# Optimization experiments

Hardware: AMD Instinct MI355X
Metric: run time of the kernel (lower is better)

Reference implementation:

```python
import jax, jax.numpy as jnp
import numpy as np

NUM_HEADS = 12
THETA = 10000.0

def apply_rope(x, pos, theta):
    # x: [B, H, S, d_k]; pos: [S]
    d_k = x.shape[-1]
    inv_freq = theta ** (-jnp.arange(0, d_k, 2, dtype=jnp.float32) / d_k)  # [d_k/2]
    ang = pos[:, None].astype(jnp.float32) * inv_freq[None, :]             # [S, d_k/2]
    cos, sin = jnp.cos(ang), jnp.sin(ang)
    x1, x2 = x[..., ::2], x[..., 1::2]
    out_even = x1 * cos - x2 * sin
    out_odd = x1 * sin + x2 * cos
    # interleave back to [..., d_k]
    return jnp.stack([out_even, out_odd], axis=-1).reshape(x.shape)

def setup_inputs() -> dict:
    key = jax.random.key(0)
    ks = jax.random.split(key, 5)
    B, S, D = 1, 4096, 768
    x = jax.random.normal(ks[0], (B, S, D), dtype=jnp.float32)
    scale = 0.02
    Wq = jax.random.normal(ks[1], (D, D), dtype=jnp.float32) * scale
    Wk = jax.random.normal(ks[2], (D, D), dtype=jnp.float32) * scale
    Wv = jax.random.normal(ks[3], (D, D), dtype=jnp.float32) * scale
    Wo = jax.random.normal(ks[4], (D, D), dtype=jnp.float32) * scale
    return {"x": x, "Wq": Wq, "Wk": Wk, "Wv": Wv, "Wo": Wo}

def reference(x, Wq, Wk, Wv, Wo):
    B, S, D = x.shape
    H = NUM_HEADS
    d_k = D // H
    # projections (torch Linear: y = x @ W.T, no bias)
    Q = x @ Wq.T
    K = x @ Wk.T
    V = x @ Wv.T
    # [B, S, H*d_k] -> [B, H, S, d_k]
    def split_heads(t):
        return t.reshape(B, S, H, d_k).transpose(0, 2, 1, 3)
    Q, K, V = split_heads(Q), split_heads(K), split_heads(V)
    pos = jnp.arange(S)
    Q = apply_rope(Q, pos, THETA)
    K = apply_rope(K, pos, THETA)
    scores = jnp.einsum('bhnd,bhmd->bhnm', Q, K) * (d_k ** -0.5)  # [B,H,S,S]
    causal = jnp.tril(jnp.ones((S, S), dtype=bool))
    scores = jnp.where(causal, scores, -jnp.inf)
    attn = jax.nn.softmax(scores, axis=-1)
    out = jnp.einsum('bhnm,bhmd->bhnd', attn, V)  # [B,H,S,d_k]
    out = out.transpose(0, 2, 1, 3).reshape(B, S, D)
    return out @ Wo.T
```

## Files before the change

kernel.cpp:

```cpp
#include <hip/hip_runtime.h>
#include <hip/hip_bf16.h>
#include <cstdint>

typedef __bf16 bf16x8 __attribute__((ext_vector_type(8)));
typedef float f32x4 __attribute__((ext_vector_type(4)));
typedef float f32x16 __attribute__((ext_vector_type(16)));

static constexpr int S = 4096;
static constexpr int D = 768;
static constexpr int DK = 64;

__device__ __forceinline__ unsigned short f2bf(float f) {
  unsigned u = __float_as_uint(f);
  u = (u + 0x7fffu + ((u >> 16) & 1u)) >> 16;
  return (unsigned short)u;
}

__global__ __launch_bounds__(256) void cvt5_kernel(
    const float* __restrict__ x, const float* __restrict__ wq,
    const float* __restrict__ wk, const float* __restrict__ wv,
    const float* __restrict__ wo,
    unsigned short* __restrict__ xb, unsigned short* __restrict__ wqb,
    unsigned short* __restrict__ wkb, unsigned short* __restrict__ wvb,
    unsigned short* __restrict__ wob, float2* __restrict__ tab) {
  int i = blockIdx.x * blockDim.x + threadIdx.x;
  constexpr int NX4 = (S * D) / 4;
  constexpr int NW4 = (D * D) / 4;
  constexpr int NC = NX4 + 4 * NW4;
  if (i < NC) {
    const float* src;
    unsigned short* dst;
    int off;
    if (i < NX4)               { src = x;  dst = xb;  off = i; }
    else if (i < NX4 + NW4)    { src = wq; dst = wqb; off = i - NX4; }
    else if (i < NX4 + 2*NW4)  { src = wk; dst = wkb; off = i - NX4 - NW4; }
    else if (i < NX4 + 3*NW4)  { src = wv; dst = wvb; off = i - NX4 - 2*NW4; }
    else                       { src = wo; dst = wob; off = i - NX4 - 3*NW4; }
    float4 v = reinterpret_cast<const float4*>(src)[off];
    ushort4 o;
    o.x = f2bf(v.x); o.y = f2bf(v.y); o.z = f2bf(v.z); o.w = f2bf(v.w);
    reinterpret_cast<ushort4*>(dst)[off] = o;
  } else {
    int idx = i - NC;
    if (idx < S * 32) {
      int s = idx >> 5, ii = idx & 31;
      float freq = expf(-(float)(2 * ii) * (9.210340371976184f / 64.0f));
      float si, c;
      sincosf((float)s * freq, &si, &c);
      tab[idx] = make_float2(c, si);
    }
  }
}

__global__ __launch_bounds__(512) void qkv_gemm_kernel(
    const unsigned short* __restrict__ xb,
    const unsigned short* __restrict__ Wall,
    const float2* __restrict__ tab,
    unsigned short* __restrict__ Qh,
    unsigned short* __restrict__ Kf,
    unsigned short* __restrict__ Vf) {
  __shared__ alignas(16) unsigned short At[2][128 * 64];
  __shared__ alignas(16) unsigned short Bt[2][128 * 64];

  const int t = threadIdx.x;
  const int lane = t & 63;
  const int lr = lane & 15;
  const int hi = lane >> 4;
  const int wave = t >> 6;
  const int wr = wave >> 1, wc = wave & 1;
  const int row0 = blockIdx.x * 128;
  const int n0 = blockIdx.y * 128;
  const int sx = lr & 7;

  f32x4 acc[2][4] = {};

  auto stage = [&](int buf, int k0) {
#pragma unroll
    for (int j = 0; j < 2; ++j) {
      const int ci = wave * 128 + j * 64 + lane;
      const int row = ci >> 3;
      const int c16 = ci & 7;
      const int csrc = (c16 ^ (row & 7)) * 8;
      __builtin_amdgcn_global_load_lds(
          (const __attribute__((address_space(1))) void*)(
              xb + (size_t)(row0 + row) * 768 + k0 + csrc),
          (__attribute__((address_space(3))) void*)(&At[buf][row * 64 + c16 * 8]),
          16, 0, 0);
      __builtin_amdgcn_global_load_lds(
          (const __attribute__((address_space(1))) void*)(
              Wall + (size_t)(n0 + row) * 768 + k0 + csrc),
          (__attribute__((address_space(3))) void*)(&Bt[buf][row * 64 + c16 * 8]),
          16, 0, 0);
    }
  };

  stage(0, 0);
  __syncthreads();

#pragma unroll
  for (int ts = 0; ts < 12; ++ts) {
    const int cur = ts & 1;
    if (ts + 1 < 12) stage(cur ^ 1, (ts + 1) * 64);
#pragma unroll
    for (int kk = 0; kk < 2; ++kk) {
      const int csw = ((kk * 4 + hi) ^ sx) * 8;
      bf16x8 a[2], b[4];
#pragma unroll
      for (int rf = 0; rf < 2; ++rf)
        a[rf] = *reinterpret_cast<const bf16x8*>(
            &At[cur][(wr * 32 + rf * 16 + lr) * 64 + csw]);
#pragma unroll
      for (int nf = 0; nf < 4; ++nf)
        b[nf] = *reinterpret_cast<const bf16x8*>(
            &Bt[cur][(wc * 64 + nf * 16 + lr) * 64 + csw]);
#pragma unroll
      for (int rf = 0; rf < 2; ++rf)
#pragma unroll
        for (int nf = 0; nf < 4; ++nf)
          acc[rf][nf] = __builtin_amdgcn_mfma_f32_16x16x32_bf16(a[rf], b[nf], acc[rf][nf], 0, 0, 0);
    }
    __syncthreads();
  }

  const int z = n0 / 768;

  if (z < 2) {
#pragma unroll
    for (int nf = 0; nf < 4; ++nf) {
      const int c = n0 - z * 768 + wc * 64 + nf * 16 + lr;
      const int hh = c >> 6;
      const int dk = c & 63;
      const int ii = dk >> 1;
#pragma unroll
      for (int rf = 0; rf < 2; ++rf) {
        const int jrow = row0 + wr * 32 + rf * 16 + hi * 4;
#pragma unroll
        for (int j = 0; j < 4; ++j) {
          float v = acc[rf][nf][j];
          const int s = jrow + j;
          float pv = __shfl_xor(v, 1);
          float2 cs = tab[(size_t)s * 32 + ii];
          v = (dk & 1) ? (pv * cs.y + v * cs.x) : (v * cs.x - pv * cs.y);
          if (z == 0) {
            Qh[((size_t)hh * S + s) * DK + dk] = f2bf(v * 0.18033688f);
          } else {
            const size_t koff = ((size_t)hh * 128 + (s >> 5)) * 2048 +
                                (size_t)(dk >> 4) * 512 + ((dk >> 3) & 1) * 256 +
                                (s & 31) * 8 + (dk & 7);
            Kf[koff] = f2bf(v);
          }
        }
      }
    }
  } else {
#pragma unroll
    for (int nf = 0; nf < 4; ++nf) {
      const int c = n0 - 1536 + wc * 64 + nf * 16 + lr;
      const int hh = c >> 6;
      const int dv = c & 63;
#pragma unroll
      for (int rf = 0; rf < 2; ++rf) {
        const int jrow = row0 + wr * 32 + rf * 16 + hi * 4;
#pragma unroll
        for (int j = 0; j < 4; ++j) {
          const int s = jrow + j;
          const size_t voff = ((size_t)hh * 256 + (s >> 4)) * 1024 +
                              (size_t)(dv >> 5) * 512 + (dv & 31) * 16 +
                              ((s >> 3) & 1) * 8 + (s & 7);
          Vf[voff] = f2bf(acc[rf][nf][j]);
        }
      }
    }
  }
}

__global__ __launch_bounds__(256) void attn_kernel(
    const unsigned short* __restrict__ Qh,
    const unsigned short* __restrict__ Kf,
    const unsigned short* __restrict__ Vf,
    unsigned short* __restrict__ AO) {
  const int c = blockIdx.x;
  const int sslot = blockIdx.y;
  const int m3 = 3 * (c >> 1);
  const int g = sslot / 3, r = sslot - 3 * g;
  int h, qt;
  if ((c & 1) == 0) {
    if (r == 0)      { h = m3;     qt = 127 - 2 * g; }
    else if (r == 1) { h = m3 + 1; qt = 127 - 2 * g; }
    else             { h = m3;     qt = 126 - 2 * g; }
  } else {
    if (r == 0)      { h = m3 + 2; qt = 127 - 2 * g; }
    else if (r == 1) { h = m3 + 2; qt = 126 - 2 * g; }
    else             { h = m3 + 1; qt = 126 - 2 * g; }
  }

  const int wave = threadIdx.x >> 6;
  const int lane = threadIdx.x & 63;
  const int lq = lane & 31;
  const int hi2 = lane >> 5;
  const int q0w = qt * 32;
  const int qg = q0w + lq;

  const unsigned short* Qp = Qh + ((size_t)h * S + qg) * DK + hi2 * 8;
  const unsigned short* Kfp = Kf + (size_t)h * (S * DK) + hi2 * 256 + lq * 8;
  const unsigned short* Vfp = Vf + (size_t)h * (S * DK) + lq * 16 + hi2 * 8;

  bf16x8 qf[4];
#pragma unroll
  for (int ks = 0; ks < 4; ++ks)
    qf[ks] = *reinterpret_cast<const bf16x8*>(Qp + ks * 16);

  f32x16 acc0 = {}, acc1 = {};
  float lsum[16];
#pragma unroll
  for (int r2 = 0; r2 < 16; ++r2) lsum[r2] = 0.f;

  const int kvmax = ((q0w + 31) >> 6) << 6;
  const int kvfirst = 64 * wave;

  bf16x8 ka[2][4];
  if (kvfirst <= kvmax) {
    const unsigned short* K0 = Kfp + ((size_t)(kvfirst >> 5)) * 2048;
#pragma unroll
    for (int tt = 0; tt < 2; ++tt)
#pragma unroll
      for (int ks = 0; ks < 4; ++ks)
        ka[tt][ks] = *reinterpret_cast<const bf16x8*>(K0 + (size_t)tt * 2048 + ks * 512);
  }

  for (int kv0 = kvfirst; kv0 <= kvmax; kv0 += 256) {
    bf16x8 vb[2][4];
#pragma unroll
    for (int dvh = 0; dvh < 2; ++dvh)
#pragma unroll
      for (int ks = 0; ks < 4; ++ks)
        vb[dvh][ks] = *reinterpret_cast<const bf16x8*>(
            Vfp + ((size_t)(kv0 >> 4) + ks) * 1024 + dvh * 512);

    f32x16 s0 = {}, s1 = {};
#pragma unroll
    for (int ks = 0; ks < 4; ++ks) {
      s0 = __builtin_amdgcn_mfma_f32_32x32x16_bf16(ka[0][ks], qf[ks], s0, 0, 0, 0);
      s1 = __builtin_amdgcn_mfma_f32_32x32x16_bf16(ka[1][ks], qf[ks], s1, 0, 0, 0);
    }

    if ((kv0 + 256) <= kvmax) {
      const unsigned short* Kn = Kfp + ((size_t)((kv0 + 256) >> 5)) * 2048;
#pragma unroll
      for (int tt = 0; tt < 2; ++tt)
#pragma unroll
        for (int ks = 0; ks < 4; ++ks)
          ka[tt][ks] = *reinterpret_cast<const bf16x8*>(Kn + (size_t)tt * 2048 + ks * 512);
    }

    if ((kv0 + 63) > q0w) {
#pragma unroll
      for (int rr = 0; rr < 16; ++rr) {
        const int kvr = kv0 + (rr & 3) + 8 * (rr >> 2) + 4 * hi2;
        if (kvr > qg) s0[rr] = -1e30f;
        if (kvr + 32 > qg) s1[rr] = -1e30f;
      }
    }

#pragma unroll
    for (int rr = 0; rr < 16; ++rr) {
      float e0, e1;
      asm("v_exp_f32 %0, %1" : "=v"(e0) : "v"(s0[rr]));
      asm("v_exp_f32 %0, %1" : "=v"(e1) : "v"(s1[rr]));
      s0[rr] = e0;
      s1[rr] = e1;
      lsum[rr] += e0 + e1;
    }

    bf16x8 pa[4];
#pragma unroll
    for (int ks = 0; ks < 4; ++ks) {
      const int a4 = 8 * (ks & 1);
      unsigned X01, X23, Y01, Y23;
      if (ks < 2) {
        asm("v_cvt_pk_bf16_f32 %0, %1, %2" : "=v"(X01) : "v"(s0[a4 + 0]), "v"(s0[a4 + 1]));
        asm("v_cvt_pk_bf16_f32 %0, %1, %2" : "=v"(X23) : "v"(s0[a4 + 2]), "v"(s0[a4 + 3]));
        asm("v_cvt_pk_bf16_f32 %0, %1, %2" : "=v"(Y01) : "v"(s0[a4 + 4]), "v"(s0[a4 + 5]));
        asm("v_cvt_pk_bf16_f32 %0, %1, %2" : "=v"(Y23) : "v"(s0[a4 + 6]), "v"(s0[a4 + 7]));
      } else {
        asm("v_cvt_pk_bf16_f32 %0, %1, %2" : "=v"(X01) : "v"(s1[a4 + 0]), "v"(s1[a4 + 1]));
        asm("v_cvt_pk_bf16_f32 %0, %1, %2" : "=v"(X23) : "v"(s1[a4 + 2]), "v"(s1[a4 + 3]));
        asm("v_cvt_pk_bf16_f32 %0, %1, %2" : "=v"(Y01) : "v"(s1[a4 + 4]), "v"(s1[a4 + 5]));
        asm("v_cvt_pk_bf16_f32 %0, %1, %2" : "=v"(Y23) : "v"(s1[a4 + 6]), "v"(s1[a4 + 7]));
      }
      asm volatile("v_permlane32_swap_b32 %0, %1" : "+v"(X01), "+v"(Y01));
      asm volatile("v_permlane32_swap_b32 %0, %1" : "+v"(X23), "+v"(Y23));
      union { unsigned u[4]; bf16x8 v; } P;
      P.u[0] = X01; P.u[1] = X23; P.u[2] = Y01; P.u[3] = Y23;
      pa[ks] = P.v;
    }

#pragma unroll
    for (int ks = 0; ks < 4; ++ks) {
      acc0 = __builtin_amdgcn_mfma_f32_32x32x16_bf16(pa[ks], vb[0][ks], acc0, 0, 0, 0);
      acc1 = __builtin_amdgcn_mfma_f32_32x32x16_bf16(pa[ks], vb[1][ks], acc1, 0, 0, 0);
    }
  }

#pragma unroll
  for (int off = 8; off > 0; off >>= 1)
#pragma unroll
    for (int rr = 0; rr < 8; ++rr)
      if (rr < off) lsum[rr] += lsum[rr + off];
  const float l_ = lsum[0] + __shfl_xor(lsum[0], 32);

  __shared__ float llds[4][32];
  __shared__ float obuf[4][64][17];

  if (hi2 == 0) llds[wave][lq] = l_;

#pragma unroll
  for (int rr = 0; rr < 16; ++rr) obuf[wave][lane][rr] = acc0[rr];
  __syncthreads();

  const float Ltot = llds[0][lq] + llds[1][lq] + llds[2][lq] + llds[3][lq];
  const float linv = 1.0f / Ltot;

  float v0[4];
#pragma unroll
  for (int rr = 0; rr < 4; ++rr) {
    const int rq = wave * 4 + rr;
    v0[rr] = obuf[0][lane][rq] + obuf[1][lane][rq] + obuf[2][lane][rq] + obuf[3][lane][rq];
  }
  __syncthreads();

#pragma unroll
  for (int rr = 0; rr < 16; ++rr) obuf[wave][lane][rr] = acc1[rr];
  __syncthreads();

#pragma unroll
  for (int rr = 0; rr < 4; ++rr) {
    const int rq = wave * 4 + rr;
    const float v1 = obuf[0][lane][rq] + obuf[1][lane][rq] + obuf[2][lane][rq] + obuf[3][lane][rq];
    const int row = (rq & 3) + 8 * (rq >> 2) + 4 * hi2;
    const float li = __shfl(linv, row);
    const size_t s = q0w + row;
    AO[s * D + h * DK + lq]      = f2bf(v0[rr] * li);
    AO[s * D + h * DK + 32 + lq] = f2bf(v1 * li);
  }
}

__global__ __launch_bounds__(256) void oproj_kernel(
    const unsigned short* __restrict__ AO,
    const unsigned short* __restrict__ Wob,
    float* __restrict__ out) {
  __shared__ alignas(16) unsigned short At[2][64 * 64];
  __shared__ alignas(16) unsigned short Bt[2][128 * 64];

  const int t = threadIdx.x;
  const int lane = t & 63;
  const int lr = lane & 15;
  const int hi = lane >> 4;
  const int wave = t >> 6;
  const int wr = wave >> 1, wc = wave & 1;
  const int row0 = blockIdx.x * 64;
  const int n0 = blockIdx.y * 128;
  const int sx = lr & 7;

  f32x4 acc[2][4] = {};

  auto stage = [&](int buf, int k0) {
#pragma unroll
    for (int p = 0; p < 2; ++p) {
      const int ci = p * 256 + t;
      const int row = ci >> 3;
      const int c16 = ci & 7;
      const int csrc = (c16 ^ (row & 7)) * 8;
      __builtin_amdgcn_global_load_lds(
          (const __attribute__((address_space(1))) void*)(
              AO + (size_t)(row0 + row) * 768 + k0 + csrc),
          (__attribute__((address_space(3))) void*)(&At[buf][row * 64 + c16 * 8]),
          16, 0, 0);
    }
#pragma unroll
    for (int p = 0; p < 4; ++p) {
      const int ci = p * 256 + t;
      const int row = ci >> 3;
      const int c16 = ci & 7;
      const int csrc = (c16 ^ (row & 7)) * 8;
      __builtin_amdgcn_global_load_lds(
          (const __attribute__((address_space(1))) void*)(
              Wob + (size_t)(n0 + row) * 768 + k0 + csrc),
          (__attribute__((address_space(3))) void*)(&Bt[buf][row * 64 + c16 * 8]),
          16, 0, 0);
    }
  };

  stage(0, 0);
  __syncthreads();

#pragma unroll
  for (int ts = 0; ts < 12; ++ts) {
    const int cur = ts & 1;
    if (ts + 1 < 12) stage(cur ^ 1, (ts + 1) * 64);
#pragma unroll
    for (int kk = 0; kk < 2; ++kk) {
      const int csw = ((kk * 4 + hi) ^ sx) * 8;
      bf16x8 a[2], b[4];
#pragma unroll
      for (int rf = 0; rf < 2; ++rf)
        a[rf] = *reinterpret_cast<const bf16x8*>(
            &At[cur][(wr * 32 + rf * 16 + lr) * 64 + csw]);
#pragma unroll
      for (int nf = 0; nf < 4; ++nf)
        b[nf] = *reinterpret_cast<const bf16x8*>(
            &Bt[cur][(wc * 64 + nf * 16 + lr) * 64 + csw]);
#pragma unroll
      for (int rf = 0; rf < 2; ++rf)
#pragma unroll
        for (int nf = 0; nf < 4; ++nf)
          acc[rf][nf] = __builtin_amdgcn_mfma_f32_16x16x32_bf16(a[rf], b[nf], acc[rf][nf], 0, 0, 0);
    }
    __syncthreads();
  }

#pragma unroll
  for (int rf = 0; rf < 2; ++rf) {
    const int jrow = row0 + wr * 32 + rf * 16 + hi * 4;
#pragma unroll
    for (int nf = 0; nf < 4; ++nf) {
      const int cn = n0 + wc * 64 + nf * 16 + lr;
#pragma unroll
      for (int j = 0; j < 4; ++j)
        out[(size_t)(jrow + j) * D + cn] = acc[rf][nf][j];
    }
  }
}

extern "C" void kernel_launch(void* const* d_in, const int* in_sizes, int n_in,
                              void* d_out, int out_size, void* d_ws, size_t ws_size,
                              hipStream_t stream) {
  const float* x  = (const float*)d_in[0];
  const float* Wq = (const float*)d_in[1];
  const float* Wk = (const float*)d_in[2];
  const float* Wv = (const float*)d_in[3];
  const float* Wo = (const float*)d_in[4];
  float* out = (float*)d_out;

  char* ws = (char*)d_ws;
  unsigned short* xb  = (unsigned short*)(ws + 0);
  unsigned short* Wqb = (unsigned short*)(ws + 6291456);
  unsigned short* Wkb = (unsigned short*)(ws + 7471104);
  unsigned short* Wvb = (unsigned short*)(ws + 8650752);
  unsigned short* Wob = (unsigned short*)(ws + 9830400);
  unsigned short* Qh  = (unsigned short*)(ws + 11010048);
  unsigned short* Kf  = (unsigned short*)(ws + 17301504);
  unsigned short* Vf  = (unsigned short*)(ws + 23592960);
  unsigned short* AO  = (unsigned short*)(ws + 29884416);
  float2* tab = (float2*)(ws + 29884416);

  cvt5_kernel<<<5888, 256, 0, stream>>>(x, Wq, Wk, Wv, Wo, xb, Wqb, Wkb, Wvb, Wob, tab);
  qkv_gemm_kernel<<<dim3(32, 18), 512, 0, stream>>>(xb, Wqb, tab, Qh, Kf, Vf);
  attn_kernel<<<dim3(8, 192), 256, 0, stream>>>(Qh, Kf, Vf, AO);
  oproj_kernel<<<dim3(64, 6), 256, 0, stream>>>(AO, Wob, out);
}
```

Before: 98.43 us.

## Share K/V tiles across waves via LDS double buffering in attention

Each attention block now covers 128 query rows, one 32-row strip per wave, instead of splitting one 32-row strip's KV range across four waves. K and V tiles are staged into LDS with global_load_lds in a double buffer, so all four waves reuse each loaded tile. This removes the cross-wave reduction of partial outputs and row sums through shared memory at the end. In exchange the grid shrinks fourfold to 384 blocks and a block barrier is added per KV tile. Causal imbalance also grows, since waves in the same block stop at different KV tiles but still wait at every barrier.

```diff
diff --git a/kernel.cpp b/kernel.cpp
--- a/kernel.cpp
+++ b/kernel.cpp
@@ -183,27 +183,30 @@
   const int sslot = blockIdx.y;
   const int m3 = 3 * (c >> 1);
   const int g = sslot / 3, r = sslot - 3 * g;
-  int h, qt;
+  int h, qb;
   if ((c & 1) == 0) {
-    if (r == 0)      { h = m3;     qt = 127 - 2 * g; }
-    else if (r == 1) { h = m3 + 1; qt = 127 - 2 * g; }
-    else             { h = m3;     qt = 126 - 2 * g; }
+    if (r == 0)      { h = m3;     qb = 31 - 2 * g; }
+    else if (r == 1) { h = m3 + 1; qb = 31 - 2 * g; }
+    else             { h = m3;     qb = 30 - 2 * g; }
   } else {
-    if (r == 0)      { h = m3 + 2; qt = 127 - 2 * g; }
-    else if (r == 1) { h = m3 + 2; qt = 126 - 2 * g; }
-    else             { h = m3 + 1; qt = 126 - 2 * g; }
+    if (r == 0)      { h = m3 + 2; qb = 31 - 2 * g; }
+    else if (r == 1) { h = m3 + 2; qb = 30 - 2 * g; }
+    else             { h = m3 + 1; qb = 30 - 2 * g; }
   }
 
   const int wave = threadIdx.x >> 6;
   const int lane = threadIdx.x & 63;
   const int lq = lane & 31;
   const int hi2 = lane >> 5;
-  const int q0w = qt * 32;
+  const int q0w = qb * 128 + wave * 32;
   const int qg = q0w + lq;
 
   const unsigned short* Qp = Qh + ((size_t)h * S + qg) * DK + hi2 * 8;
-  const unsigned short* Kfp = Kf + (size_t)h * (S * DK) + hi2 * 256 + lq * 8;
-  const unsigned short* Vfp = Vf + (size_t)h * (S * DK) + lq * 16 + hi2 * 8;
+  const unsigned short* Kfp = Kf + (size_t)h * (S * DK);
+  const unsigned short* Vfp = Vf + (size_t)h * (S * DK);
+
+  __shared__ alignas(16) unsigned short Kt[2][4096];
+  __shared__ alignas(16) unsigned short Vt[2][4096];
 
   bf16x8 qf[4];
 #pragma unroll
@@ -215,91 +218,102 @@
 #pragma unroll
   for (int r2 = 0; r2 < 16; ++r2) lsum[r2] = 0.f;
 
-  const int kvmax = ((q0w + 31) >> 6) << 6;
-  const int kvfirst = 64 * wave;
-
-  bf16x8 ka[2][4];
-  if (kvfirst <= kvmax) {
-    const unsigned short* K0 = Kfp + ((size_t)(kvfirst >> 5)) * 2048;
-#pragma unroll
-    for (int tt = 0; tt < 2; ++tt)
-#pragma unroll
-      for (int ks = 0; ks < 4; ++ks)
-        ka[tt][ks] = *reinterpret_cast<const bf16x8*>(K0 + (size_t)tt * 2048 + ks * 512);
-  }
-
-  for (int kv0 = kvfirst; kv0 <= kvmax; kv0 += 256) {
-    bf16x8 vb[2][4];
-#pragma unroll
-    for (int dvh = 0; dvh < 2; ++dvh)
-#pragma unroll
-      for (int ks = 0; ks < 4; ++ks)
-        vb[dvh][ks] = *reinterpret_cast<const bf16x8*>(
-            Vfp + ((size_t)(kv0 >> 4) + ks) * 1024 + dvh * 512);
-
-    f32x16 s0 = {}, s1 = {};
-#pragma unroll
-    for (int ks = 0; ks < 4; ++ks) {
-      s0 = __builtin_amdgcn_mfma_f32_32x32x16_bf16(ka[0][ks], qf[ks], s0, 0, 0, 0);
-      s1 = __builtin_amdgcn_mfma_f32_32x32x16_bf16(ka[1][ks], qf[ks], s1, 0, 0, 0);
-    }
-
-    if ((kv0 + 256) <= kvmax) {
-      const unsigned short* Kn = Kfp + ((size_t)((kv0 + 256) >> 5)) * 2048;
-#pragma unroll
-      for (int tt = 0; tt < 2; ++tt)
+  const int ntiles = 2 * qb + 2;
+
+  auto stage = [&](int buf, int t2) {
+    const unsigned short* Ksrc = Kfp + (size_t)t2 * 4096;
+    const unsigned short* Vsrc = Vfp + (size_t)t2 * 4096;
+#pragma unroll
+    for (int p = 0; p < 2; ++p) {
+      const int ci = wave * 128 + p * 64 + lane;
+      __builtin_amdgcn_global_load_lds(
+          (const __attribute__((address_space(1))) void*)(Ksrc + ci * 8),
+          (__attribute__((address_space(3))) void*)(&Kt[buf][ci * 8]), 16, 0, 0);
+      __builtin_amdgcn_global_load_lds(
+          (const __attribute__((address_space(1))) void*)(Vsrc + ci * 8),
+          (__attribute__((address_space(3))) void*)(&Vt[buf][ci * 8]), 16, 0, 0);
+    }
+  };
+
+  stage(0, 0);
+  __syncthreads();
+
+  for (int tt = 0; tt < ntiles; ++tt) {
+    const int cur = tt & 1;
+    if (tt + 1 < ntiles) stage(cur ^ 1, tt + 1);
+
+    const int kv0 = 64 * tt;
+    if (kv0 <= q0w + 31) {
+      bf16x8 ka[2][4], vb[2][4];
+#pragma unroll
+      for (int t2 = 0; t2 < 2; ++t2)
 #pragma unroll
         for (int ks = 0; ks < 4; ++ks)
-          ka[tt][ks] = *reinterpret_cast<const bf16x8*>(Kn + (size_t)tt * 2048 + ks * 512);
-    }
-
-    if ((kv0 + 63) > q0w) {
+          ka[t2][ks] = *reinterpret_cast<const bf16x8*>(
+              &Kt[cur][t2 * 2048 + ks * 512 + hi2 * 256 + lq * 8]);
+#pragma unroll
+      for (int dvh = 0; dvh < 2; ++dvh)
+#pragma unroll
+        for (int ks = 0; ks < 4; ++ks)
+          vb[dvh][ks] = *reinterpret_cast<const bf16x8*>(
+              &Vt[cur][ks * 1024 + dvh * 512 + lq * 16 + hi2 * 8]);
+
+      f32x16 s0 = {}, s1 = {};
+#pragma unroll
+      for (int ks = 0; ks < 4; ++ks) {
+        s0 = __builtin_amdgcn_mfma_f32_32x32x16_bf16(ka[0][ks], qf[ks], s0, 0, 0, 0);
+        s1 = __builtin_amdgcn_mfma_f32_32x32x16_bf16(ka[1][ks], qf[ks], s1, 0, 0, 0);
+      }
+
+      if ((kv0 + 63) > q0w) {
+#pragma unroll
+        for (int rr = 0; rr < 16; ++rr) {
+          const int kvr = kv0 + (rr & 3) + 8 * (rr >> 2) + 4 * hi2;
+          if (kvr > qg) s0[rr] = -1e30f;
+          if (kvr + 32 > qg) s1[rr] = -1e30f;
+        }
+      }
+
 #pragma unroll
       for (int rr = 0; rr < 16; ++rr) {
-        const int kvr = kv0 + (rr & 3) + 8 * (rr >> 2) + 4 * hi2;
-        if (kvr > qg) s0[rr] = -1e30f;
-        if (kvr + 32 > qg) s1[rr] = -1e30f;
-      }
-    }
-
-#pragma unroll
-    for (int rr = 0; rr < 16; ++rr) {
-      float e0, e1;
-      asm("v_exp_f32 %0, %1" : "=v"(e0) : "v"(s0[rr]));
-      asm("v_exp_f32 %0, %1" : "=v"(e1) : "v"(s1[rr]));
-      s0[rr] = e0;
-      s1[rr] = e1;
-      lsum[rr] += e0 + e1;
-    }
-
-    bf16x8 pa[4];
-#pragma unroll
-    for (int ks = 0; ks < 4; ++ks) {
-      const int a4 = 8 * (ks & 1);
-      unsigned X01, X23, Y01, Y23;
-      if (ks < 2) {
-        asm("v_cvt_pk_bf16_f32 %0, %1, %2" : "=v"(X01) : "v"(s0[a4 + 0]), "v"(s0[a4 + 1]));
-        asm("v_cvt_pk_bf16_f32 %0, %1, %2" : "=v"(X23) : "v"(s0[a4 + 2]), "v"(s0[a4 + 3]));
-        asm("v_cvt_pk_bf16_f32 %0, %1, %2" : "=v"(Y01) : "v"(s0[a4 + 4]), "v"(s0[a4 + 5]));
-        asm("v_cvt_pk_bf16_f32 %0, %1, %2" : "=v"(Y23) : "v"(s0[a4 + 6]), "v"(s0[a4 + 7]));
-      } else {
-        asm("v_cvt_pk_bf16_f32 %0, %1, %2" : "=v"(X01) : "v"(s1[a4 + 0]), "v"(s1[a4 + 1]));
-        asm("v_cvt_pk_bf16_f32 %0, %1, %2" : "=v"(X23) : "v"(s1[a4 + 2]), "v"(s1[a4 + 3]));
-        asm("v_cvt_pk_bf16_f32 %0, %1, %2" : "=v"(Y01) : "v"(s1[a4 + 4]), "v"(s1[a4 + 5]));
-        asm("v_cvt_pk_bf16_f32 %0, %1, %2" : "=v"(Y23) : "v"(s1[a4 + 6]), "v"(s1[a4 + 7]));
-      }
-      asm volatile("v_permlane32_swap_b32 %0, %1" : "+v"(X01), "+v"(Y01));
-      asm volatile("v_permlane32_swap_b32 %0, %1" : "+v"(X23), "+v"(Y23));
-      union { unsigned u[4]; bf16x8 v; } P;
-      P.u[0] = X01; P.u[1] = X23; P.u[2] = Y01; P.u[3] = Y23;
-      pa[ks] = P.v;
-    }
-
-#pragma unroll
-    for (int ks = 0; ks < 4; ++ks) {
-      acc0 = __builtin_amdgcn_mfma_f32_32x32x16_bf16(pa[ks], vb[0][ks], acc0, 0, 0, 0);
-      acc1 = __builtin_amdgcn_mfma_f32_32x32x16_bf16(pa[ks], vb[1][ks], acc1, 0, 0, 0);
-    }
+        float e0, e1;
+        asm("v_exp_f32 %0, %1" : "=v"(e0) : "v"(s0[rr]));
+        asm("v_exp_f32 %0, %1" : "=v"(e1) : "v"(s1[rr]));
+        s0[rr] = e0;
+        s1[rr] = e1;
+        lsum[rr] += e0 + e1;
+      }
+
+      bf16x8 pa[4];
+#pragma unroll
+      for (int ks = 0; ks < 4; ++ks) {
+        const int a4 = 8 * (ks & 1);
+        unsigned X01, X23, Y01, Y23;
+        if (ks < 2) {
+          asm("v_cvt_pk_bf16_f32 %0, %1, %2" : "=v"(X01) : "v"(s0[a4 + 0]), "v"(s0[a4 + 1]));
+          asm("v_cvt_pk_bf16_f32 %0, %1, %2" : "=v"(X23) : "v"(s0[a4 + 2]), "v"(s0[a4 + 3]));
+          asm("v_cvt_pk_bf16_f32 %0, %1, %2" : "=v"(Y01) : "v"(s0[a4 + 4]), "v"(s0[a4 + 5]));
+          asm("v_cvt_pk_bf16_f32 %0, %1, %2" : "=v"(Y23) : "v"(s0[a4 + 6]), "v"(s0[a4 + 7]));
+        } else {
+          asm("v_cvt_pk_bf16_f32 %0, %1, %2" : "=v"(X01) : "v"(s1[a4 + 0]), "v"(s1[a4 + 1]));
+          asm("v_cvt_pk_bf16_f32 %0, %1, %2" : "=v"(X23) : "v"(s1[a4 + 2]), "v"(s1[a4 + 3]));
+          asm("v_cvt_pk_bf16_f32 %0, %1, %2" : "=v"(Y01) : "v"(s1[a4 + 4]), "v"(s1[a4 + 5]));
+          asm("v_cvt_pk_bf16_f32 %0, %1, %2" : "=v"(Y23) : "v"(s1[a4 + 6]), "v"(s1[a4 + 7]));
+        }
+        asm volatile("v_permlane32_swap_b32 %0, %1" : "+v"(X01), "+v"(Y01));
+        asm volatile("v_permlane32_swap_b32 %0, %1" : "+v"(X23), "+v"(Y23));
+        union { unsigned u[4]; bf16x8 v; } P;
+        P.u[0] = X01; P.u[1] = X23; P.u[2] = Y01; P.u[3] = Y23;
+        pa[ks] = P.v;
+      }
+
+#pragma unroll
+      for (int ks = 0; ks < 4; ++ks) {
+        acc0 = __builtin_amdgcn_mfma_f32_32x32x16_bf16(pa[ks], vb[0][ks], acc0, 0, 0, 0);
+        acc1 = __builtin_amdgcn_mfma_f32_32x32x16_bf16(pa[ks], vb[1][ks], acc1, 0, 0, 0);
+      }
+    }
+    __syncthreads();
   }
 
 #pragma unroll
@@ -308,40 +322,15 @@
     for (int rr = 0; rr < 8; ++rr)
       if (rr < off) lsum[rr] += lsum[rr + off];
   const float l_ = lsum[0] + __shfl_xor(lsum[0], 32);
-
-  __shared__ float llds[4][32];
-  __shared__ float obuf[4][64][17];
-
-  if (hi2 == 0) llds[wave][lq] = l_;
-
-#pragma unroll
-  for (int rr = 0; rr < 16; ++rr) obuf[wave][lane][rr] = acc0[rr];
-  __syncthreads();
-
-  const float Ltot = llds[0][lq] + llds[1][lq] + llds[2][lq] + llds[3][lq];
-  const float linv = 1.0f / Ltot;
-
-  float v0[4];
-#pragma unroll
-  for (int rr = 0; rr < 4; ++rr) {
-    const int rq = wave * 4 + rr;
-    v0[rr] = obuf[0][lane][rq] + obuf[1][lane][rq] + obuf[2][lane][rq] + obuf[3][lane][rq];
-  }
-  __syncthreads();
-
-#pragma unroll
-  for (int rr = 0; rr < 16; ++rr) obuf[wave][lane][rr] = acc1[rr];
-  __syncthreads();
-
-#pragma unroll
-  for (int rr = 0; rr < 4; ++rr) {
-    const int rq = wave * 4 + rr;
-    const float v1 = obuf[0][lane][rq] + obuf[1][lane][rq] + obuf[2][lane][rq] + obuf[3][lane][rq];
-    const int row = (rq & 3) + 8 * (rq >> 2) + 4 * hi2;
+  const float linv = 1.0f / l_;
+
+#pragma unroll
+  for (int rr = 0; rr < 16; ++rr) {
+    const int row = (rr & 3) + 8 * (rr >> 2) + 4 * hi2;
     const float li = __shfl(linv, row);
     const size_t s = q0w + row;
-    AO[s * D + h * DK + lq]      = f2bf(v0[rr] * li);
-    AO[s * D + h * DK + 32 + lq] = f2bf(v1 * li);
+    AO[s * D + h * DK + lq]      = f2bf(acc0[rr] * li);
+    AO[s * D + h * DK + 32 + lq] = f2bf(acc1[rr] * li);
   }
 }
 
@@ -456,6 +445,6 @@
 
   cvt5_kernel<<<5888, 256, 0, stream>>>(x, Wq, Wk, Wv, Wo, xb, Wqb, Wkb, Wvb, Wob, tab);
   qkv_gemm_kernel<<<dim3(32, 18), 512, 0, stream>>>(xb, Wqb, tab, Qh, Kf, Vf);
-  attn_kernel<<<dim3(8, 192), 256, 0, stream>>>(Qh, Kf, Vf, AO);
+  attn_kernel<<<dim3(8, 48), 256, 0, stream>>>(Qh, Kf, Vf, AO);
   oproj_kernel<<<dim3(64, 6), 256, 0, stream>>>(AO, Wob, out);
 }
```

Result: slower. 136.9 us (+39.1%).
